# Optimization experiments

Measured on AMD Instinct MI355X. Metric: run time of the kernel, lower is better.

Reference implementation:

```python
import jax, jax.numpy as jnp
import numpy as np

B, N, TOP_K = 4, 2048, 30
NUM_PE, NUM_RBF, EDGE_F = 16, 16, 128

def l2norm(x, eps=1e-12):
    return x / jnp.maximum(jnp.linalg.norm(x, axis=-1, keepdims=True), eps)

def gather_nodes(nodes, idx):
    # nodes [B,N,C], idx [B,N,K] -> [B,N,K,C]
    return jax.vmap(lambda n, i: n[i])(nodes, idx)

def setup_inputs() -> dict:
    key = jax.random.key(0)
    k1, k2 = jax.random.split(key)
    X = jax.random.normal(k1, (B, N, 3), dtype=jnp.float32) * 5.0
    mask = jnp.ones((B, N), dtype=jnp.float32)
    W = jax.random.normal(k2, (NUM_PE + NUM_RBF + 7, EDGE_F), dtype=jnp.float32) * 0.1
    b = jnp.zeros((EDGE_F,), dtype=jnp.float32)
    gamma = jnp.ones((EDGE_F,), dtype=jnp.float32)
    beta = jnp.zeros((EDGE_F,), dtype=jnp.float32)
    return {"X": X, "mask": mask, "W": W, "b": b, "gamma": gamma, "beta": beta}

def _quaternions(R):
    # R [B,N,K,3,3] -> Q [B,N,K,4]
    diag = jnp.diagonal(R, axis1=-2, axis2=-1)  # [B,N,K,3]
    Rxx, Ryy, Rzz = diag[..., 0], diag[..., 1], diag[..., 2]
    mags = 0.5 * jnp.sqrt(jnp.abs(1.0 + jnp.stack(
        [Rxx - Ryy - Rzz, -Rxx + Ryy - Rzz, -Rxx - Ryy + Rzz], -1)))
    signs = jnp.sign(jnp.stack([
        R[..., 2, 1] - R[..., 1, 2],
        R[..., 0, 2] - R[..., 2, 0],
        R[..., 1, 0] - R[..., 0, 1]], -1))
    xyz = signs * mags
    w = jnp.sqrt(jax.nn.relu(1.0 + jnp.sum(diag, -1, keepdims=True))) / 2.0
    Q = jnp.concatenate((xyz, w), -1)
    return l2norm(Q)

def _forward(X, mask, W, b, gamma, beta):
    eps = 1e-6
    # pairwise distances + top-k neighbors
    mask_2D = mask[:, None, :] * mask[:, :, None]
    dXp = X[:, None, :, :] - X[:, :, None, :]
    D = mask_2D * jnp.sqrt(jnp.sum(dXp ** 2, -1) + eps)
    D_max = jnp.max(D, -1, keepdims=True)
    D_adjust = D + (1.0 - mask_2D) * D_max
    neg_vals, E_idx = jax.lax.top_k(-D_adjust, TOP_K)
    D_neighbors = -neg_vals

    # RBF
    D_mu = jnp.linspace(0.0, 20.0, NUM_RBF)
    D_sigma = 20.0 / NUM_RBF
    RBF = jnp.exp(-(((D_neighbors[..., None] - D_mu) / D_sigma) ** 2))

    # orientations
    dX = X[:, 1:, :] - X[:, :-1, :]
    U = l2norm(dX)
    u_2, u_1 = U[:, :-2, :], U[:, 1:-1, :]
    n_2 = l2norm(jnp.cross(u_2, u_1))
    o_1 = l2norm(u_2 - u_1)
    O = jnp.stack((o_1, n_2, jnp.cross(o_1, n_2)), 2)  # [B,N-3,3,3]
    O9 = O.reshape(O.shape[0], O.shape[1], 9)
    O9 = jnp.pad(O9, ((0, 0), (1, 2), (0, 0)))  # [B,N,9]
    O_neighbors = gather_nodes(O9, E_idx).reshape(B, N, TOP_K, 3, 3)
    X_neighbors = gather_nodes(X, E_idx)  # [B,N,K,3]
    Om = O9.reshape(B, N, 3, 3)
    dXn = X_neighbors - X[:, :, None, :]
    dU = l2norm(jnp.einsum('bnij,bnkj->bnki', Om, dXn))
    R = jnp.einsum('bnji,bnkjl->bnkil', Om, O_neighbors)
    Q = _quaternions(R)
    O_features = jnp.concatenate((dU, Q), -1)  # [B,N,K,7]

    # positional encodings
    ii = jnp.arange(N, dtype=jnp.float32)[None, :, None]
    d = (E_idx.astype(jnp.float32) - ii)[..., None]
    freq = jnp.exp(jnp.arange(0, NUM_PE, 2, dtype=jnp.float32) * -(np.log(10000.0) / NUM_PE))
    angles = d * freq
    E_positional = jnp.concatenate((jnp.cos(angles), jnp.sin(angles)), -1)

    E = jnp.concatenate((E_positional, RBF, O_features), -1)  # [B,N,K,39]
    E = E @ W + b
    # Normalize (LayerNorm w/ unbiased std, as in struct2seq Normalize)
    mu = jnp.mean(E, -1, keepdims=True)
    sigma = jnp.sqrt(jnp.var(E, -1, keepdims=True, ddof=1) + eps)
    E = gamma * (E - mu) / (sigma + eps) + beta
    return E, E_idx

def reference(X, mask, W, b, gamma, beta):
    return _forward(X, mask, W, b, gamma, beta)
```

## Files before the change

kernel.cpp:

```cpp
#include <hip/hip_runtime.h>
#include <stdint.h>

#define B_ 4
#define N_ 2048
#define K_ 30
#define F_ 128
#define NF 39

typedef unsigned long long u64;
typedef float f32x4 __attribute__((ext_vector_type(4)));
typedef short s16x8 __attribute__((ext_vector_type(8)));

__device__ __forceinline__ u64 umin64(u64 a, u64 b) { return a < b ? a : b; }

template <int CTRL>
__device__ __forceinline__ float dpp_add(float x) {
    int r = __builtin_amdgcn_update_dpp(0, __float_as_int(x), CTRL, 0xF, 0xF, true);
    return x + __int_as_float(r);
}
__device__ __forceinline__ float rowsum16(float x) {
    x = dpp_add<0xB1>(x);
    x = dpp_add<0x4E>(x);
    x = dpp_add<0x141>(x);
    x = dpp_add<0x140>(x);
    return x;
}

__device__ __forceinline__ unsigned int bf16rne(float f) {
    unsigned int u = __float_as_uint(f);
    return (u + 0x7FFFu + ((u >> 16) & 1u)) >> 16;
}
__device__ __forceinline__ unsigned int bfpack(float a, float b) {
    return bf16rne(a) | (bf16rne(b) << 16);
}

__global__ __launch_bounds__(256) void frames_kernel(const float* __restrict__ X,
                                                     float* __restrict__ O9) {
    int g = blockIdx.x * blockDim.x + threadIdx.x;
    if (g >= B_ * N_) return;
    int i = g % N_;
    float o[9] = {0.f,0.f,0.f,0.f,0.f,0.f,0.f,0.f,0.f};
    if (i >= 1 && i <= N_ - 3) {
        const float* Xp = X + (size_t)(g - i) * 3;
        float ax = Xp[3*(i-1)],   ay = Xp[3*(i-1)+1], az = Xp[3*(i-1)+2];
        float bx = Xp[3*i],       by = Xp[3*i+1],     bz = Xp[3*i+2];
        float cx = Xp[3*(i+1)],   cy = Xp[3*(i+1)+1], cz = Xp[3*(i+1)+2];
        float u2x = bx-ax, u2y = by-ay, u2z = bz-az;
        float n2_ = sqrtf(u2x*u2x+u2y*u2y+u2z*u2z);
        float inv = 1.0f / fmaxf(n2_, 1e-12f);
        u2x*=inv; u2y*=inv; u2z*=inv;
        float u1x = cx-bx, u1y = cy-by, u1z = cz-bz;
        float n1_ = sqrtf(u1x*u1x+u1y*u1y+u1z*u1z);
        inv = 1.0f / fmaxf(n1_, 1e-12f);
        u1x*=inv; u1y*=inv; u1z*=inv;
        float nx = u2y*u1z - u2z*u1y;
        float ny = u2z*u1x - u2x*u1z;
        float nz = u2x*u1y - u2y*u1x;
        float nn = sqrtf(nx*nx+ny*ny+nz*nz);
        inv = 1.0f / fmaxf(nn, 1e-12f);
        nx*=inv; ny*=inv; nz*=inv;
        float ox = u2x-u1x, oy = u2y-u1y, oz = u2z-u1z;
        float no = sqrtf(ox*ox+oy*oy+oz*oz);
        inv = 1.0f / fmaxf(no, 1e-12f);
        ox*=inv; oy*=inv; oz*=inv;
        float ccx = oy*nz - oz*ny;
        float ccy = oz*nx - ox*nz;
        float ccz = ox*ny - oy*nx;
        o[0]=ox; o[1]=oy; o[2]=oz;
        o[3]=nx; o[4]=ny; o[5]=nz;
        o[6]=ccx; o[7]=ccy; o[8]=ccz;
    }
    float* dst = O9 + (size_t)g * 9;
    #pragma unroll
    for (int q = 0; q < 9; ++q) dst[q] = o[q];
}

__global__ __launch_bounds__(256) void topk_kernel(const float* __restrict__ X,
                                                   int* __restrict__ Eidx,
                                                   float* __restrict__ Dn,
                                                   float* __restrict__ EidxF) {
    __shared__ float xs[N_], ys[N_], zs[N_];
    __shared__ u64 surv[4][64];
    int t = threadIdx.x, lane = t & 63, wid = t >> 6;
    int node = blockIdx.x * 4 + wid;
    int b = node >> 11, i = node & (N_ - 1);
    const float* Xb = X + (size_t)b * N_ * 3;

    for (int idx = t; idx < 3 * N_; idx += 256) {
        float v = Xb[idx];
        int j = idx / 3, c = idx - 3 * j;
        if (c == 0) xs[j] = v; else if (c == 1) ys[j] = v; else zs[j] = v;
    }
    __syncthreads();

    float xi = xs[i], yi = ys[i], zi = zs[i];

    unsigned int d[32];
    #pragma unroll
    for (int s = 0; s < 32; ++s) {
        int j = lane + (s << 6);
        float dx = __fsub_rn(xs[j], xi);
        float dy = __fsub_rn(ys[j], yi);
        float dz = __fsub_rn(zs[j], zi);
        float s1 = __fadd_rn(__fmul_rn(dx,dx), __fmul_rn(dy,dy));
        float s2 = __fadd_rn(s1, __fmul_rn(dz,dz));
        float ssq = __fadd_rn(s2, 1e-6f);
        d[s] = __float_as_uint(__fsqrt_rn(ssq));
    }

    unsigned int lm = d[0];
    #pragma unroll
    for (int s = 1; s < 32; ++s) lm = min(lm, d[s]);

    unsigned int v = lm;
    #pragma unroll
    for (int k = 2; k <= 64; k <<= 1) {
        #pragma unroll
        for (int j = k >> 1; j >= 1; j >>= 1) {
            unsigned int o = (unsigned int)__shfl_xor((int)v, j, 64);
            bool up = ((lane & k) == 0);
            bool lower = ((lane & j) == 0);
            v = (lower == up) ? min(v, o) : max(v, o);
        }
    }
    unsigned int Bcut = (unsigned int)__shfl((int)v, K_ - 1, 64);

    int base = 0;
    #pragma unroll
    for (int s = 0; s < 32; ++s) {
        bool p = (d[s] <= Bcut);
        u64 blt = __ballot(p);
        if (p) {
            int slot = base + (int)__popcll(blt & ((1ull << lane) - 1ull));
            if (slot < 64)
                surv[wid][slot] = (((u64)d[s]) << 32) | (unsigned int)(lane + (s << 6));
        }
        base += (int)__popcll(blt);
    }
    __syncthreads();
    int cnt = base;

    if (cnt <= 64) {
        u64 mykey = (lane < cnt) ? surv[wid][lane] : ~0ull;
        int rank = 0;
        for (int r = 0; r < cnt; ++r) {
            u64 kr = __shfl(mykey, r, 64);
            rank += (kr < mykey) ? 1 : 0;
        }
        if (lane < cnt && rank < K_) {
            int j = (int)(mykey & 0xffffffffull);
            int o = node * K_ + rank;
            Eidx[o] = j;
            Dn[o] = __uint_as_float((unsigned int)(mykey >> 32));
            EidxF[o] = (float)j;
        }
    } else {
        for (int k = 0; k < K_; ++k) {
            u64 m = ~0ull;
            #pragma unroll
            for (int s = 0; s < 32; ++s) {
                u64 kk = (((u64)d[s]) << 32) | (unsigned int)(lane + (s << 6));
                m = umin64(m, kk);
            }
            #pragma unroll
            for (int off = 1; off < 64; off <<= 1)
                m = umin64(m, (u64)__shfl_xor(m, off, 64));
            #pragma unroll
            for (int s = 0; s < 32; ++s) {
                u64 kk = (((u64)d[s]) << 32) | (unsigned int)(lane + (s << 6));
                if (kk == m) d[s] = 0xFFFFFFFFu;
            }
            if (lane == 0) {
                int o = node * K_ + k;
                int j = (int)(m & 0xffffffffull);
                Eidx[o] = j;
                Dn[o] = __uint_as_float((unsigned int)(m >> 32));
                EidxF[o] = (float)j;
            }
        }
    }
}

__global__ __launch_bounds__(256) void edge_fused(const float* __restrict__ X,
                                                  const float* __restrict__ O9,
                                                  const int* __restrict__ Eidx,
                                                  const float* __restrict__ Dn,
                                                  const float* __restrict__ W,
                                                  const float* __restrict__ bias,
                                                  const float* __restrict__ gamma,
                                                  const float* __restrict__ beta,
                                                  float* __restrict__ E) {
    __shared__ unsigned int ldsF[128 * 32];
    __shared__ unsigned int ldsW[128 * 32];
    int t = threadIdx.x, lane = t & 63, wid = t >> 6;
    int e0 = blockIdx.x * 128;

    if (t < 128) {
        int e = e0 + t;
        int b = e / (N_ * K_);
        int rem = e - b * (N_ * K_);
        int i = rem / K_;
        int node = b * N_ + i;
        int j = Eidx[e];
        float dnb = Dn[e];

        float f[40];
        float dd = (float)(j - i);
        const float freqs[8] = {1.0f, 0.31622776601683794f, 0.1f, 0.031622776601683794f,
                                0.01f, 0.0031622776601683794f, 0.001f, 0.00031622776601683794f};
        #pragma unroll
        for (int l = 0; l < 8; ++l) {
            float a = dd * freqs[l];
            float sv, cv;
            __sincosf(a, &sv, &cv);
            f[l] = cv;
            f[8 + l] = sv;
        }
        #pragma unroll
        for (int r = 0; r < 16; ++r) {
            float mu = (20.0f / 15.0f) * (float)r;
            float u = (dnb - mu) * 0.8f;
            f[16 + r] = __expf(-u * u);
        }
        const float* Omp = O9 + (size_t)node * 9;
        float Om[9];
        #pragma unroll
        for (int q = 0; q < 9; ++q) Om[q] = Omp[q];
        const float* Xi = X + (size_t)node * 3;
        const float* Xj = X + (size_t)(b * N_ + j) * 3;
        float dx = Xj[0] - Xi[0], dy = Xj[1] - Xi[1], dz = Xj[2] - Xi[2];
        float v0 = Om[0]*dx + Om[1]*dy + Om[2]*dz;
        float v1 = Om[3]*dx + Om[4]*dy + Om[5]*dz;
        float v2 = Om[6]*dx + Om[7]*dy + Om[8]*dz;
        float n = sqrtf(v0*v0 + v1*v1 + v2*v2);
        float inv = 1.0f / fmaxf(n, 1e-12f);
        f[32] = v0 * inv; f[33] = v1 * inv; f[34] = v2 * inv;
        const float* On = O9 + (size_t)(b * N_ + j) * 9;
        float R00 = Om[0]*On[0] + Om[3]*On[3] + Om[6]*On[6];
        float R01 = Om[0]*On[1] + Om[3]*On[4] + Om[6]*On[7];
        float R02 = Om[0]*On[2] + Om[3]*On[5] + Om[6]*On[8];
        float R10 = Om[1]*On[0] + Om[4]*On[3] + Om[7]*On[6];
        float R11 = Om[1]*On[1] + Om[4]*On[4] + Om[7]*On[7];
        float R12 = Om[1]*On[2] + Om[4]*On[5] + Om[7]*On[8];
        float R20 = Om[2]*On[0] + Om[5]*On[3] + Om[8]*On[6];
        float R21 = Om[2]*On[1] + Om[5]*On[4] + Om[8]*On[7];
        float R22 = Om[2]*On[2] + Om[5]*On[5] + Om[8]*On[8];
        float mg0 = 0.5f * sqrtf(fabsf(1.0f + R00 - R11 - R22));
        float mg1 = 0.5f * sqrtf(fabsf(1.0f - R00 + R11 - R22));
        float mg2 = 0.5f * sqrtf(fabsf(1.0f - R00 - R11 + R22));
        float t0 = R21 - R12, t1 = R02 - R20, t2 = R10 - R01;
        float s0 = (t0 > 0.f) ? 1.f : ((t0 < 0.f) ? -1.f : 0.f);
        float s1 = (t1 > 0.f) ? 1.f : ((t1 < 0.f) ? -1.f : 0.f);
        float s2 = (t2 > 0.f) ? 1.f : ((t2 < 0.f) ? -1.f : 0.f);
        float q0 = s0 * mg0, q1 = s1 * mg1, q2 = s2 * mg2;
        float w = sqrtf(fmaxf(1.0f + R00 + R11 + R22, 0.0f)) * 0.5f;
        float nq = sqrtf(q0*q0 + q1*q1 + q2*q2 + w*w);
        inv = 1.0f / fmaxf(nq, 1e-12f);
        f[35] = q0 * inv; f[36] = q1 * inv; f[37] = q2 * inv; f[38] = w * inv;
        f[39] = 0.0f;

        int row = t;
        #pragma unroll
        for (int c = 0; c < 8; ++c) {
            uint4 u;
            if (c < 5) {
                u.x = bfpack(f[8*c+0], f[8*c+1]);
                u.y = bfpack(f[8*c+2], f[8*c+3]);
                u.z = bfpack(f[8*c+4], f[8*c+5]);
                u.w = bfpack(f[8*c+6], f[8*c+7]);
            } else {
                u = make_uint4(0u, 0u, 0u, 0u);
            }
            int idx = row * 32 + ((4 * c) ^ ((row & 7) << 2));
            *(uint4*)&ldsF[idx] = u;
        }
    } else {
        unsigned short* ws = (unsigned short*)ldsW;
        int col = t - 128;
        #pragma unroll
        for (int r = 0; r < 64; ++r) {
            unsigned short v = (r < NF) ? (unsigned short)bf16rne(W[r * F_ + col])
                                        : (unsigned short)0;
            ws[col * 64 + (r ^ ((col & 7) << 3))] = v;
        }
    }

    float gg[8], be8[8], bb[8];
    #pragma unroll
    for (int tt = 0; tt < 8; ++tt) {
        int c = 16 * tt + (lane & 15);
        gg[tt] = gamma[c]; be8[tt] = beta[c]; bb[tt] = bias[c];
    }

    __syncthreads();

    s16x8 wf[8][2];
    #pragma unroll
    for (int tt = 0; tt < 8; ++tt) {
        int col = 16 * tt + (lane & 15);
        #pragma unroll
        for (int s = 0; s < 2; ++s) {
            int idx = col * 32 + ((((lane >> 4) * 4) + s * 16) ^ ((col & 7) << 2));
            wf[tt][s] = *(s16x8*)&ldsW[idx];
        }
    }

    #pragma unroll
    for (int wt = 0; wt < 2; ++wt) {
        int ebase = wid * 32 + wt * 16;
        int arow = ebase + (lane & 15);
        s16x8 af[2];
        #pragma unroll
        for (int s = 0; s < 2; ++s) {
            int idx = arow * 32 + ((((lane >> 4) * 4) + s * 16) ^ ((arow & 7) << 2));
            af[s] = *(s16x8*)&ldsF[idx];
        }
        f32x4 acc[8];
        #pragma unroll
        for (int tt = 0; tt < 8; ++tt) {
            acc[tt] = (f32x4){0.f, 0.f, 0.f, 0.f};
            acc[tt] = __builtin_amdgcn_mfma_f32_16x16x32_bf16(af[0], wf[tt][0], acc[tt], 0, 0, 0);
            acc[tt] = __builtin_amdgcn_mfma_f32_16x16x32_bf16(af[1], wf[tt][1], acc[tt], 0, 0, 0);
        }
        float sum[4] = {0,0,0,0}, sq[4] = {0,0,0,0};
        #pragma unroll
        for (int tt = 0; tt < 8; ++tt) {
            #pragma unroll
            for (int q = 0; q < 4; ++q) {
                float v = acc[tt][q] + bb[tt];
                acc[tt][q] = v;
                sum[q] += v;
                sq[q] = fmaf(v, v, sq[q]);
            }
        }
        float muv[4], invv[4];
        #pragma unroll
        for (int q = 0; q < 4; ++q) {
            float S  = rowsum16(sum[q]);
            float Qs = rowsum16(sq[q]);
            float mu = S * (1.0f / 128.0f);
            float var = (Qs - S * mu) * (1.0f / 127.0f);
            muv[q] = mu;
            invv[q] = 1.0f / (sqrtf(var + 1e-6f) + 1e-6f);
        }
        size_t base = (size_t)(e0 + ebase) * F_;
        #pragma unroll
        for (int tt = 0; tt < 8; ++tt) {
            int c = 16 * tt + (lane & 15);
            #pragma unroll
            for (int q = 0; q < 4; ++q) {
                int er = (lane >> 4) * 4 + q;
                E[base + (size_t)er * F_ + c] =
                    gg[tt] * (acc[tt][q] - muv[q]) * invv[q] + be8[tt];
            }
        }
    }
}

extern "C" void kernel_launch(void* const* d_in, const int* in_sizes, int n_in,
                              void* d_out, int out_size, void* d_ws, size_t ws_size,
                              hipStream_t stream) {
    const float* X     = (const float*)d_in[0];
    const float* W     = (const float*)d_in[2];
    const float* bias  = (const float*)d_in[3];
    const float* gamma = (const float*)d_in[4];
    const float* beta  = (const float*)d_in[5];

    float* E      = (float*)d_out;
    float* EidxF  = (float*)d_out + (size_t)B_ * N_ * K_ * F_;

    float* O9   = (float*)d_ws;
    int*   Eidx = (int*)(O9 + (size_t)B_ * N_ * 9);
    float* Dn   = (float*)(Eidx + (size_t)B_ * N_ * K_);

    int nodes = B_ * N_;
    int edges = nodes * K_;

    hipLaunchKernelGGL(frames_kernel, dim3((nodes + 255) / 256), dim3(256), 0, stream,
                       X, O9);
    hipLaunchKernelGGL(topk_kernel, dim3(nodes / 4), dim3(256), 0, stream,
                       X, Eidx, Dn, EidxF);
    hipLaunchKernelGGL(edge_fused, dim3(edges / 128), dim3(256), 0, stream,
                       X, O9, Eidx, Dn, W, bias, gamma, beta, E);
}
```

Measured before the change: 57.17 us.

## Fuse frame computation into top-k kernel and defer sqrt to survivors

Drops the separate frames kernel: the top-k block computes the orientation frames for its four nodes from the coordinates already staged in LDS, saving a launch. Coordinates are stored as float4 so each neighbour needs one LDS load. Ranking uses squared distances, with sqrt taken only for survivors (the cutoff gets a small ulp margin), and the O(n^2) rank count becomes a bitonic sort over 64 keys. The W staging writes packed 16-byte bf16 vectors instead of scalar shorts. The ulp-widened cutoff and squared-distance comparison could change tie ordering or overflow the survivor buffer more often, sending more nodes to the slow fallback.

```diff
diff --git a/kernel.cpp b/kernel.cpp
--- a/kernel.cpp
+++ b/kernel.cpp
@@ -12,6 +12,7 @@
 typedef short s16x8 __attribute__((ext_vector_type(8)));
 
 __device__ __forceinline__ u64 umin64(u64 a, u64 b) { return a < b ? a : b; }
+__device__ __forceinline__ u64 umax64(u64 a, u64 b) { return a > b ? a : b; }
 
 template <int CTRL>
 __device__ __forceinline__ float dpp_add(float x) {
@@ -34,97 +35,92 @@
     return bf16rne(a) | (bf16rne(b) << 16);
 }
 
-__global__ __launch_bounds__(256) void frames_kernel(const float* __restrict__ X,
-                                                     float* __restrict__ O9) {
-    int g = blockIdx.x * blockDim.x + threadIdx.x;
-    if (g >= B_ * N_) return;
-    int i = g % N_;
-    float o[9] = {0.f,0.f,0.f,0.f,0.f,0.f,0.f,0.f,0.f};
-    if (i >= 1 && i <= N_ - 3) {
-        const float* Xp = X + (size_t)(g - i) * 3;
-        float ax = Xp[3*(i-1)],   ay = Xp[3*(i-1)+1], az = Xp[3*(i-1)+2];
-        float bx = Xp[3*i],       by = Xp[3*i+1],     bz = Xp[3*i+2];
-        float cx = Xp[3*(i+1)],   cy = Xp[3*(i+1)+1], cz = Xp[3*(i+1)+2];
-        float u2x = bx-ax, u2y = by-ay, u2z = bz-az;
-        float n2_ = sqrtf(u2x*u2x+u2y*u2y+u2z*u2z);
-        float inv = 1.0f / fmaxf(n2_, 1e-12f);
-        u2x*=inv; u2y*=inv; u2z*=inv;
-        float u1x = cx-bx, u1y = cy-by, u1z = cz-bz;
-        float n1_ = sqrtf(u1x*u1x+u1y*u1y+u1z*u1z);
-        inv = 1.0f / fmaxf(n1_, 1e-12f);
-        u1x*=inv; u1y*=inv; u1z*=inv;
-        float nx = u2y*u1z - u2z*u1y;
-        float ny = u2z*u1x - u2x*u1z;
-        float nz = u2x*u1y - u2y*u1x;
-        float nn = sqrtf(nx*nx+ny*ny+nz*nz);
-        inv = 1.0f / fmaxf(nn, 1e-12f);
-        nx*=inv; ny*=inv; nz*=inv;
-        float ox = u2x-u1x, oy = u2y-u1y, oz = u2z-u1z;
-        float no = sqrtf(ox*ox+oy*oy+oz*oz);
-        inv = 1.0f / fmaxf(no, 1e-12f);
-        ox*=inv; oy*=inv; oz*=inv;
-        float ccx = oy*nz - oz*ny;
-        float ccy = oz*nx - ox*nz;
-        float ccz = ox*ny - oy*nx;
-        o[0]=ox; o[1]=oy; o[2]=oz;
-        o[3]=nx; o[4]=ny; o[5]=nz;
-        o[6]=ccx; o[7]=ccy; o[8]=ccz;
-    }
-    float* dst = O9 + (size_t)g * 9;
-    #pragma unroll
-    for (int q = 0; q < 9; ++q) dst[q] = o[q];
-}
-
 __global__ __launch_bounds__(256) void topk_kernel(const float* __restrict__ X,
+                                                   float* __restrict__ O9,
                                                    int* __restrict__ Eidx,
                                                    float* __restrict__ Dn,
                                                    float* __restrict__ EidxF) {
-    __shared__ float xs[N_], ys[N_], zs[N_];
+    __shared__ float4 P[N_];
     __shared__ u64 surv[4][64];
     int t = threadIdx.x, lane = t & 63, wid = t >> 6;
     int node = blockIdx.x * 4 + wid;
-    int b = node >> 11, i = node & (N_ - 1);
-    const float* Xb = X + (size_t)b * N_ * 3;
+    int i = node & (N_ - 1);
+    const float* Xb = X + (size_t)(node - i) * 3;
+    float* Pf = (float*)P;
 
     for (int idx = t; idx < 3 * N_; idx += 256) {
         float v = Xb[idx];
         int j = idx / 3, c = idx - 3 * j;
-        if (c == 0) xs[j] = v; else if (c == 1) ys[j] = v; else zs[j] = v;
+        Pf[4 * j + c] = v;
     }
     __syncthreads();
 
-    float xi = xs[i], yi = ys[i], zi = zs[i];
+    if (t < 4) {
+        int nn = blockIdx.x * 4 + t;
+        int ii = nn & (N_ - 1);
+        float o[9] = {0.f,0.f,0.f,0.f,0.f,0.f,0.f,0.f,0.f};
+        if (ii >= 1 && ii <= N_ - 3) {
+            float4 A = P[ii-1], Bv = P[ii], C = P[ii+1];
+            float u2x = Bv.x-A.x, u2y = Bv.y-A.y, u2z = Bv.z-A.z;
+            float n2_ = sqrtf(u2x*u2x+u2y*u2y+u2z*u2z);
+            float inv = 1.0f / fmaxf(n2_, 1e-12f);
+            u2x*=inv; u2y*=inv; u2z*=inv;
+            float u1x = C.x-Bv.x, u1y = C.y-Bv.y, u1z = C.z-Bv.z;
+            float n1_ = sqrtf(u1x*u1x+u1y*u1y+u1z*u1z);
+            inv = 1.0f / fmaxf(n1_, 1e-12f);
+            u1x*=inv; u1y*=inv; u1z*=inv;
+            float nx = u2y*u1z - u2z*u1y;
+            float ny = u2z*u1x - u2x*u1z;
+            float nz = u2x*u1y - u2y*u1x;
+            float nn2 = sqrtf(nx*nx+ny*ny+nz*nz);
+            inv = 1.0f / fmaxf(nn2, 1e-12f);
+            nx*=inv; ny*=inv; nz*=inv;
+            float ox = u2x-u1x, oy = u2y-u1y, oz = u2z-u1z;
+            float no = sqrtf(ox*ox+oy*oy+oz*oz);
+            inv = 1.0f / fmaxf(no, 1e-12f);
+            ox*=inv; oy*=inv; oz*=inv;
+            o[0]=ox; o[1]=oy; o[2]=oz;
+            o[3]=nx; o[4]=ny; o[5]=nz;
+            o[6]=oy*nz - oz*ny; o[7]=oz*nx - ox*nz; o[8]=ox*ny - oy*nx;
+        }
+        float* dst = O9 + (size_t)nn * 9;
+        #pragma unroll
+        for (int q = 0; q < 9; ++q) dst[q] = o[q];
+    }
+
+    float4 ci = P[i];
+    float xi = ci.x, yi = ci.y, zi = ci.z;
 
     unsigned int d[32];
     #pragma unroll
     for (int s = 0; s < 32; ++s) {
-        int j = lane + (s << 6);
-        float dx = __fsub_rn(xs[j], xi);
-        float dy = __fsub_rn(ys[j], yi);
-        float dz = __fsub_rn(zs[j], zi);
+        float4 p = P[lane + (s << 6)];
+        float dx = __fsub_rn(p.x, xi);
+        float dy = __fsub_rn(p.y, yi);
+        float dz = __fsub_rn(p.z, zi);
         float s1 = __fadd_rn(__fmul_rn(dx,dx), __fmul_rn(dy,dy));
         float s2 = __fadd_rn(s1, __fmul_rn(dz,dz));
-        float ssq = __fadd_rn(s2, 1e-6f);
-        d[s] = __float_as_uint(__fsqrt_rn(ssq));
+        d[s] = __float_as_uint(__fadd_rn(s2, 1e-6f));
     }
 
     unsigned int lm = d[0];
     #pragma unroll
     for (int s = 1; s < 32; ++s) lm = min(lm, d[s]);
 
-    unsigned int v = lm;
+    unsigned int v32 = lm;
     #pragma unroll
     for (int k = 2; k <= 64; k <<= 1) {
         #pragma unroll
         for (int j = k >> 1; j >= 1; j >>= 1) {
-            unsigned int o = (unsigned int)__shfl_xor((int)v, j, 64);
+            unsigned int o = (unsigned int)__shfl_xor((int)v32, j, 64);
             bool up = ((lane & k) == 0);
             bool lower = ((lane & j) == 0);
-            v = (lower == up) ? min(v, o) : max(v, o);
-        }
-    }
-    unsigned int Bcut = (unsigned int)__shfl((int)v, K_ - 1, 64);
-
+            v32 = (lower == up) ? min(v32, o) : max(v32, o);
+        }
+    }
+    unsigned int Bcut = (unsigned int)__shfl((int)v32, K_ - 1, 64) + 64u;
+
+    surv[wid][lane] = ~0ull;
     int base = 0;
     #pragma unroll
     for (int s = 0; s < 32; ++s) {
@@ -132,29 +128,39 @@
         u64 blt = __ballot(p);
         if (p) {
             int slot = base + (int)__popcll(blt & ((1ull << lane) - 1ull));
-            if (slot < 64)
-                surv[wid][slot] = (((u64)d[s]) << 32) | (unsigned int)(lane + (s << 6));
+            if (slot < 64) {
+                float D = __fsqrt_rn(__uint_as_float(d[s]));
+                surv[wid][slot] = (((u64)__float_as_uint(D)) << 32)
+                                | (unsigned int)(lane + (s << 6));
+            }
         }
         base += (int)__popcll(blt);
     }
-    __syncthreads();
     int cnt = base;
 
     if (cnt <= 64) {
-        u64 mykey = (lane < cnt) ? surv[wid][lane] : ~0ull;
-        int rank = 0;
-        for (int r = 0; r < cnt; ++r) {
-            u64 kr = __shfl(mykey, r, 64);
-            rank += (kr < mykey) ? 1 : 0;
-        }
-        if (lane < cnt && rank < K_) {
-            int j = (int)(mykey & 0xffffffffull);
-            int o = node * K_ + rank;
+        u64 v = surv[wid][lane];
+        #pragma unroll
+        for (int k = 2; k <= 64; k <<= 1) {
+            #pragma unroll
+            for (int j = k >> 1; j >= 1; j >>= 1) {
+                u64 o = (u64)__shfl_xor((long long)v, j, 64);
+                bool up = ((lane & k) == 0);
+                bool lower = ((lane & j) == 0);
+                v = (lower == up) ? umin64(v, o) : umax64(v, o);
+            }
+        }
+        if (lane < K_ && lane < cnt) {
+            int j = (int)(v & 0xffffffffull);
+            int o = node * K_ + lane;
             Eidx[o] = j;
-            Dn[o] = __uint_as_float((unsigned int)(mykey >> 32));
+            Dn[o] = __uint_as_float((unsigned int)(v >> 32));
             EidxF[o] = (float)j;
         }
     } else {
+        #pragma unroll
+        for (int s = 0; s < 32; ++s)
+            d[s] = __float_as_uint(__fsqrt_rn(__uint_as_float(d[s])));
         for (int k = 0; k < K_; ++k) {
             u64 m = ~0ull;
             #pragma unroll
@@ -164,7 +170,7 @@
             }
             #pragma unroll
             for (int off = 1; off < 64; off <<= 1)
-                m = umin64(m, (u64)__shfl_xor(m, off, 64));
+                m = umin64(m, (u64)__shfl_xor((long long)m, off, 64));
             #pragma unroll
             for (int s = 0; s < 32; ++s) {
                 u64 kk = (((u64)d[s]) << 32) | (unsigned int)(lane + (s << 6));
@@ -275,13 +281,20 @@
             *(uint4*)&ldsF[idx] = u;
         }
     } else {
-        unsigned short* ws = (unsigned short*)ldsW;
         int col = t - 128;
         #pragma unroll
-        for (int r = 0; r < 64; ++r) {
-            unsigned short v = (r < NF) ? (unsigned short)bf16rne(W[r * F_ + col])
-                                        : (unsigned short)0;
-            ws[col * 64 + (r ^ ((col & 7) << 3))] = v;
+        for (int c8 = 0; c8 < 8; ++c8) {
+            uint4 u;
+            unsigned int* up = (unsigned int*)&u;
+            #pragma unroll
+            for (int m = 0; m < 4; ++m) {
+                int k0 = 8 * c8 + 2 * m, k1 = k0 + 1;
+                float a  = (k0 < NF) ? W[k0 * F_ + col] : 0.f;
+                float bv = (k1 < NF) ? W[k1 * F_ + col] : 0.f;
+                up[m] = bfpack(a, bv);
+            }
+            int idx = col * 32 + ((4 * c8) ^ ((col & 7) << 2));
+            *(uint4*)&ldsW[idx] = u;
         }
     }
 
@@ -376,10 +389,8 @@
     int nodes = B_ * N_;
     int edges = nodes * K_;
 
-    hipLaunchKernelGGL(frames_kernel, dim3((nodes + 255) / 256), dim3(256), 0, stream,
-                       X, O9);
     hipLaunchKernelGGL(topk_kernel, dim3(nodes / 4), dim3(256), 0, stream,
-                       X, Eidx, Dn, EidxF);
+                       X, O9, Eidx, Dn, EidxF);
     hipLaunchKernelGGL(edge_fused, dim3(edges / 128), dim3(256), 0, stream,
                        X, O9, Eidx, Dn, W, bias, gamma, beta, E);
 }
```

After: 51.01 us. -10.8%, faster.
